# Optimization experiments

Measured on AMD Instinct MI355X. Metric: run time of the kernel, lower is better.

The kernel has to match this reference:

```python
import jax, jax.numpy as jnp
import numpy as np

DIM = 1024          # moe_cfg.dim
INTER = 1024        # moe_cfg.moe_inter_dim
E = 8               # moe_cfg.n_routed_experts
TOPK = 2            # moe_cfg.n_activated_experts
ROUTE_SCALE = 1.0
SHARED_INTER = 2048 # n_shared_experts * moe_inter_dim
B, S = 4, 2048


def setup_inputs() -> dict:
    key = jax.random.key(0)
    ks = jax.random.split(key, 10)
    def w(k, shape, scale=0.02):
        return jax.random.normal(k, shape, jnp.float32) * scale
    return {
        "x": jax.random.normal(ks[0], (B, S, DIM), jnp.float32),
        # Gate (nn.Linear(dim, n_routed_experts, bias=True))
        "gate_w": w(ks[1], (E, DIM)),
        "gate_b": jnp.zeros((E,), jnp.float32),
        # Routed experts, stacked on leading E axis (torch Linear convention: [out, in])
        "w1": w(ks[2], (E, INTER, DIM)), "b1": jnp.zeros((E, INTER), jnp.float32),
        "w3": w(ks[3], (E, INTER, DIM)), "b3": jnp.zeros((E, INTER), jnp.float32),
        "w2": w(ks[4], (E, DIM, INTER)), "b2": jnp.zeros((E, DIM), jnp.float32),
        # Shared expert MLP(dim, n_shared_experts * moe_inter_dim)
        "ws1": w(ks[5], (SHARED_INTER, DIM)), "bs1": jnp.zeros((SHARED_INTER,), jnp.float32),
        "ws3": w(ks[6], (SHARED_INTER, DIM)), "bs3": jnp.zeros((SHARED_INTER,), jnp.float32),
        "ws2": w(ks[7], (DIM, SHARED_INTER)), "bs2": jnp.zeros((DIM,), jnp.float32),
    }


def _moe_forward(x, gate_w, gate_b, w1, b1, w3, b3, w2, b2,
                 ws1, bs1, ws3, bs3, ws2, bs2):
    Bq, Sq, D = x.shape
    xt = x.reshape(-1, D)  # [T, D], T = B*S
    # ---- Gate: softmax scores in fp32, top-k routing (eval mode: no usage buffers) ----
    logits = (xt @ gate_w.T + gate_b).astype(jnp.float32)  # [T, E]
    scores = jax.nn.softmax(logits, axis=-1)
    top_w, top_i = jax.lax.top_k(scores, TOPK)             # values == gathered scores
    weights = (top_w * ROUTE_SCALE).astype(x.dtype)        # [T, topk]
    # Dense combine weights [T, E]: zero for unrouted experts (math identical to dispatch)
    gate_dense = jnp.sum(jax.nn.one_hot(top_i, E, dtype=x.dtype) * weights[..., None], axis=1)
    # ---- Routed experts: SwiGLU FFN per expert (dropout p=0 -> identity) ----
    def expert(w1e, b1e, w3e, b3e, w2e, b2e):
        h = jax.nn.silu(xt @ w1e.T + b1e) * (xt @ w3e.T + b3e)  # [T, INTER]
        return h @ w2e.T + b2e                                   # [T, D]
    outs = jax.vmap(expert)(w1, b1, w3, b3, w2, b2)  # [E, T, D]
    y = jnp.einsum('etd,te->td', outs, gate_dense)   # weighted combine
    # ---- Shared expert MLP (SwiGLU) ----
    z = (jax.nn.silu(xt @ ws1.T + bs1) * (xt @ ws3.T + bs3)) @ ws2.T + bs2
    return (y + z).reshape(Bq, Sq, D)


def reference(x, gate_w, gate_b, w1, b1, w3, b3, w2, b2,
              ws1, bs1, ws3, bs3, ws2, bs2):
    return _moe_forward(x, gate_w, gate_b, w1, b1, w3, b3, w2, b2,
                        ws1, bs1, ws3, bs3, ws2, bs2)
```

## Files before the change

kernel.cpp:

```cpp
#include <hip/hip_runtime.h>
#include <stdint.h>
#include <stddef.h>

#define T_TOK  8192
#define DIMK   1024
#define INTERK 1024
#define NEXP   8
#define SINT   2048
#define CAP    18432
#define RT256  72

typedef float  f32x4  __attribute__((ext_vector_type(4)));
typedef short  bf16x8 __attribute__((ext_vector_type(8)));

typedef __attribute__((address_space(1))) const unsigned int gas_u32;
typedef __attribute__((address_space(3))) unsigned int las_u32;

__device__ __forceinline__ void gload16(const void* g, void* l) {
  __builtin_amdgcn_global_load_lds((gas_u32*)g, (las_u32*)l, 16, 0, 0);
}

__device__ __forceinline__ unsigned short f2b(float f) {
  unsigned int u = __float_as_uint(f);
  u = (u + 0x7FFFu + ((u >> 16) & 1u)) >> 16;
  return (unsigned short)u;
}
__device__ __forceinline__ float b2f(unsigned short h) {
  return __uint_as_float(((unsigned int)h) << 16);
}

__device__ __forceinline__ void barrier_nodrain() {
  asm volatile("" ::: "memory");
  __builtin_amdgcn_s_barrier();
  asm volatile("" ::: "memory");
}

__global__ __launch_bounds__(256) void cvt_kernel(const float4* __restrict__ in,
                                                  unsigned short* __restrict__ out, int n4) {
  int i = blockIdx.x * 256 + threadIdx.x;
  if (i >= n4) return;
  float4 v = in[i];
  ushort4 o;
  o.x = f2b(v.x); o.y = f2b(v.y); o.z = f2b(v.z); o.w = f2b(v.w);
  *reinterpret_cast<ushort4*>(&out[(size_t)i * 4]) = o;
}

template <int ROWS_PER_E, int K4>
__global__ __launch_bounds__(256) void cvt_w13_kernel(
    const float4* __restrict__ w1, const float4* __restrict__ w3,
    unsigned short* __restrict__ out, int n ) {
  int idx = blockIdx.x * 256 + threadIdx.x;
  int is3 = idx >= n;
  int i = is3 ? idx - n : idx;
  if (i >= n) return;
  int r  = i / K4;
  int kc = i - r * K4;
  int e  = r / ROWS_PER_E;
  int rr = r - e * ROWS_PER_E;
  int g  = rr >> 4;
  size_t dst_r = (size_t)e * (2 * ROWS_PER_E) + g * 32 + (is3 ? 16 : 0) + (rr & 15);
  float4 v = (is3 ? w3 : w1)[i];
  ushort4 o;
  o.x = f2b(v.x); o.y = f2b(v.y); o.z = f2b(v.z); o.w = f2b(v.w);
  *reinterpret_cast<ushort4*>(&out[(dst_r * K4 + kc) * 4]) = o;
}

__global__ __launch_bounds__(256) void gate_kernel(
    const float* __restrict__ x, const float* __restrict__ gw, const float* __restrict__ gb,
    int* __restrict__ top_i, float* __restrict__ top_w) {
  int t    = blockIdx.x * 4 + (threadIdx.x >> 6);
  int lane = threadIdx.x & 63;
  const float* xr = x + (size_t)t * DIMK;
  float acc[NEXP];
#pragma unroll
  for (int e = 0; e < NEXP; ++e) acc[e] = 0.f;
  for (int i = lane; i < DIMK; i += 64) {
    float xv = xr[i];
#pragma unroll
    for (int e = 0; e < NEXP; ++e) acc[e] += xv * gw[e * DIMK + i];
  }
#pragma unroll
  for (int e = 0; e < NEXP; ++e) {
    float v = acc[e];
#pragma unroll
    for (int off = 32; off > 0; off >>= 1) v += __shfl_down(v, off, 64);
    acc[e] = v;
  }
  if (lane == 0) {
    float lg[NEXP];
#pragma unroll
    for (int e = 0; e < NEXP; ++e) lg[e] = acc[e] + gb[e];
    int i0 = 0;
#pragma unroll
    for (int e = 1; e < NEXP; ++e) if (lg[e] > lg[i0]) i0 = e;
    int i1 = (i0 == 0) ? 1 : 0;
#pragma unroll
    for (int e = 0; e < NEXP; ++e) if (e != i0 && lg[e] > lg[i1]) i1 = e;
    float mx = lg[i0], s = 0.f;
#pragma unroll
    for (int e = 0; e < NEXP; ++e) s += expf(lg[e] - mx);
    top_i[t * 2]     = i0;
    top_i[t * 2 + 1] = i1;
    top_w[t * 2]     = expf(lg[i0] - mx) / s;
    top_w[t * 2 + 1] = expf(lg[i1] - mx) / s;
  }
}

__global__ __launch_bounds__(512) void route_build_kernel(
    const int* __restrict__ top_i, int* __restrict__ order, int* __restrict__ pos,
    int* __restrict__ poff_g) {
  __shared__ int cnt[NEXP][512];
  __shared__ int base[NEXP][512];
  __shared__ int totals[NEXP];
  __shared__ int poff_s[NEXP + 1];
  int tid = threadIdx.x;
  int lane = tid & 63, w = tid >> 6;
  const int t0 = tid * 16;

  int c[NEXP];
#pragma unroll
  for (int e = 0; e < NEXP; ++e) c[e] = 0;
  for (int j = 0; j < 16; ++j) {
    int e0 = top_i[(t0 + j) * 2];
    int e1 = top_i[(t0 + j) * 2 + 1];
#pragma unroll
    for (int e = 0; e < NEXP; ++e) c[e] += (e0 == e) + (e1 == e);
  }
#pragma unroll
  for (int e = 0; e < NEXP; ++e) cnt[e][tid] = c[e];
  __syncthreads();

  {
    int running = 0;
    for (int ch = 0; ch < 8; ++ch) {
      int v = cnt[w][ch * 64 + lane];
      int incl = v;
#pragma unroll
      for (int off = 1; off < 64; off <<= 1) {
        int u = __shfl_up(incl, off, 64);
        if (lane >= off) incl += u;
      }
      base[w][ch * 64 + lane] = running + incl - v;
      running += __shfl(incl, 63, 64);
    }
    if (lane == 0) totals[w] = running;
  }
  __syncthreads();

  if (tid == 0) {
    int off = 0;
#pragma unroll
    for (int e = 0; e < NEXP; ++e) {
      poff_s[e] = off;
      off += (totals[e] + 255) & ~255;
    }
    poff_s[NEXP] = off;
#pragma unroll
    for (int e = 0; e <= NEXP; ++e) poff_g[e] = poff_s[e];
  }
  __syncthreads();

  int cur[NEXP];
#pragma unroll
  for (int e = 0; e < NEXP; ++e) cur[e] = poff_s[e] + base[e][tid];
  for (int j = 0; j < 16; ++j) {
    int t = t0 + j;
#pragma unroll
    for (int k = 0; k < 2; ++k) {
      int ei = top_i[t * 2 + k];
      int p = 0;
#pragma unroll
      for (int e = 0; e < NEXP; ++e)
        if (ei == e) { p = cur[e]; cur[e] = p + 1; }
      order[p]       = t;
      pos[t * 2 + k] = p;
    }
  }

#pragma unroll
  for (int e = 0; e < NEXP; ++e) {
    int s = poff_s[e] + totals[e], en = poff_s[e + 1];
    for (int i = s + tid; i < en; i += 512) order[i] = 0;
  }
}

#define A_ELE   16384
#define B_ELE   8192
#define BUF_ELE (A_ELE + B_ELE)
template <bool EXPERTS, bool GATHER, int EPI>
__global__ __launch_bounds__(512) void gemm256_kernel(
    const unsigned short* __restrict__ A, int lda,
    const int* __restrict__ order, const int* __restrict__ poff,
    const unsigned short* __restrict__ B,
    const float* __restrict__ bias1, const float* __restrict__ bias3,
    size_t wstride, int bstride, int K,
    void* __restrict__ outp, int ldo) {
  __shared__ unsigned short lds[3 * BUF_ELE];

  int rowbase = blockIdx.y * 256;
  int expert  = 0;
  if (EXPERTS) {
    if (rowbase >= poff[NEXP]) return;
    while (expert < NEXP - 1 && rowbase >= poff[expert + 1]) ++expert;
  }
  const unsigned short* Be = B + (size_t)expert * wstride;

  int tid = threadIdx.x;
  int lane = tid & 63, wid = tid >> 6;
  int wr = wid >> 1, wc = wid & 1;
  int ncolbase = blockIdx.x * 128;

  size_t aoff[4], boff[2];
#pragma unroll
  for (int l = 0; l < 4; ++l) {
    int g = l * 512 + tid;
    int r = g >> 3;
    int sub = (g & 7) ^ (r & 7);
    int gr = GATHER ? order[rowbase + r] : (rowbase + r);
    aoff[l] = (size_t)gr * lda + (size_t)(sub * 8);
  }
#pragma unroll
  for (int l = 0; l < 2; ++l) {
    int g = l * 512 + tid;
    int r = g >> 3;
    int sub = (g & 7) ^ (r & 7);
    boff[l] = (size_t)(ncolbase + r) * K + (size_t)(sub * 8);
  }

  f32x4 acc[4][4];
#pragma unroll
  for (int m = 0; m < 4; ++m)
#pragma unroll
    for (int n = 0; n < 4; ++n) acc[m][n] = f32x4{0.f, 0.f, 0.f, 0.f};

  const int NT = K >> 6;

#pragma unroll
  for (int l = 0; l < 4; ++l)
    gload16(A + aoff[l], &lds[(size_t)(l * 512 + tid) * 8]);
#pragma unroll
  for (int l = 0; l < 2; ++l)
    gload16(Be + boff[l], &lds[A_ELE + (size_t)(l * 512 + tid) * 8]);
#pragma unroll
  for (int l = 0; l < 4; ++l)
    gload16(A + aoff[l] + 64, &lds[BUF_ELE + (size_t)(l * 512 + tid) * 8]);
#pragma unroll
  for (int l = 0; l < 2; ++l)
    gload16(Be + boff[l] + 64, &lds[BUF_ELE + A_ELE + (size_t)(l * 512 + tid) * 8]);

  unsigned int off_r = 0, off_m = BUF_ELE, off_w = 2 * BUF_ELE;

  for (int t = 0; t < NT; ++t) {
    if (t + 1 < NT) {
      asm volatile("s_waitcnt vmcnt(6)" ::: "memory");
    } else {
      asm volatile("s_waitcnt vmcnt(0)" ::: "memory");
    }
    asm volatile("s_waitcnt lgkmcnt(0)" ::: "memory");
    barrier_nodrain();

    const unsigned short* Ab = &lds[off_r];
    const unsigned short* Bb = &lds[off_r + A_ELE];
    const bool stage = (t + 2 < NT);
    const int kb = (t + 2) << 6;

    {
      bf16x8 a[4], b[4];
#pragma unroll
      for (int m = 0; m < 4; ++m) {
        int ra = wr * 64 + m * 16 + (lane & 15);
        int sa = ((lane >> 4)) ^ (ra & 7);
        a[m] = *(const bf16x8*)&Ab[ra * 64 + sa * 8];
      }
#pragma unroll
      for (int n = 0; n < 4; ++n) {
        int rb = wc * 64 + n * 16 + (lane & 15);
        int sb = ((lane >> 4)) ^ (rb & 7);
        b[n] = *(const bf16x8*)&Bb[rb * 64 + sb * 8];
      }
      if (stage) {
#pragma unroll
        for (int l = 0; l < 4; ++l)
          gload16(A + aoff[l] + kb, &lds[off_w + (size_t)(l * 512 + tid) * 8]);
      }
      __builtin_amdgcn_s_setprio(1);
#pragma unroll
      for (int m = 0; m < 4; ++m)
#pragma unroll
        for (int n = 0; n < 4; ++n)
          acc[m][n] = __builtin_amdgcn_mfma_f32_16x16x32_bf16(a[m], b[n], acc[m][n], 0, 0, 0);
      __builtin_amdgcn_s_setprio(0);
    }
    {
      bf16x8 a[4], b[4];
#pragma unroll
      for (int m = 0; m < 4; ++m) {
        int ra = wr * 64 + m * 16 + (lane & 15);
        int sa = (4 + (lane >> 4)) ^ (ra & 7);
        a[m] = *(const bf16x8*)&Ab[ra * 64 + sa * 8];
      }
#pragma unroll
      for (int n = 0; n < 4; ++n) {
        int rb = wc * 64 + n * 16 + (lane & 15);
        int sb = (4 + (lane >> 4)) ^ (rb & 7);
        b[n] = *(const bf16x8*)&Bb[rb * 64 + sb * 8];
      }
      if (stage) {
#pragma unroll
        for (int l = 0; l < 2; ++l)
          gload16(Be + boff[l] + kb, &lds[off_w + A_ELE + (size_t)(l * 512 + tid) * 8]);
      }
      __builtin_amdgcn_s_setprio(1);
#pragma unroll
      for (int m = 0; m < 4; ++m)
#pragma unroll
        for (int n = 0; n < 4; ++n)
          acc[m][n] = __builtin_amdgcn_mfma_f32_16x16x32_bf16(a[m], b[n], acc[m][n], 0, 0, 0);
      __builtin_amdgcn_s_setprio(0);
    }

    unsigned int tmp = off_r; off_r = off_m; off_m = off_w; off_w = tmp;
  }

  if (EPI == 0) {
#pragma unroll
    for (int m = 0; m < 4; ++m)
#pragma unroll
      for (int np = 0; np < 2; ++np) {
        int realcol = (ncolbase >> 1) + wc * 32 + np * 16 + (lane & 15);
        float bb1 = bias1[bstride * expert + realcol];
        float bb3 = bias3[bstride * expert + realcol];
#pragma unroll
        for (int j = 0; j < 4; ++j) {
          int row  = rowbase + wr * 64 + m * 16 + (lane >> 4) * 4 + j;
          float a1 = acc[m][2 * np][j] + bb1;
          float a3 = acc[m][2 * np + 1][j] + bb3;
          float hv = (a1 / (1.f + __expf(-a1))) * a3;
          ((unsigned short*)outp)[(size_t)row * ldo + realcol] = f2b(hv);
        }
      }
  } else {
#pragma unroll
    for (int m = 0; m < 4; ++m)
#pragma unroll
      for (int n = 0; n < 4; ++n) {
        int col  = ncolbase + wc * 64 + n * 16 + (lane & 15);
        float bb = bias1[bstride * expert + col];
#pragma unroll
        for (int j = 0; j < 4; ++j) {
          int row = rowbase + wr * 64 + m * 16 + (lane >> 4) * 4 + j;
          float v = acc[m][n][j] + bb;
          if (EPI == 2)
            ((float*)outp)[(size_t)row * ldo + col] = v;
          else
            ((unsigned short*)outp)[(size_t)row * ldo + col] = f2b(v);
        }
      }
  }
}

__global__ __launch_bounds__(256) void combine_kernel(
    float* __restrict__ out, const unsigned short* __restrict__ y,
    const int* __restrict__ pos, const float* __restrict__ tw) {
  size_t idx = (size_t)blockIdx.x * 256 + threadIdx.x;
  if (idx >= (size_t)T_TOK * DIMK) return;
  int t = (int)(idx >> 10);
  int d = (int)(idx & 1023);
  int p0 = pos[t * 2], p1 = pos[t * 2 + 1];
  float w0 = tw[t * 2], w1 = tw[t * 2 + 1];
  out[idx] += w0 * b2f(y[(size_t)p0 * DIMK + d]) + w1 * b2f(y[(size_t)p1 * DIMK + d]);
}

extern "C" void kernel_launch(void* const* d_in, const int* in_sizes, int n_in,
                              void* d_out, int out_size, void* d_ws, size_t ws_size,
                              hipStream_t stream) {
  const float* x   = (const float*)d_in[0];
  const float* gw  = (const float*)d_in[1];
  const float* gb  = (const float*)d_in[2];
  const float* w1  = (const float*)d_in[3];
  const float* b1  = (const float*)d_in[4];
  const float* w3  = (const float*)d_in[5];
  const float* b3  = (const float*)d_in[6];
  const float* w2  = (const float*)d_in[7];
  const float* b2  = (const float*)d_in[8];
  const float* ws1 = (const float*)d_in[9];
  const float* bs1 = (const float*)d_in[10];
  const float* ws3 = (const float*)d_in[11];
  const float* bs3 = (const float*)d_in[12];
  const float* ws2 = (const float*)d_in[13];
  const float* bs2 = (const float*)d_in[14];
  float* out = (float*)d_out;
  (void)in_sizes; (void)n_in; (void)out_size; (void)ws_size;

  char* p = (char*)d_ws;
  auto alloc = [&](size_t bytes) -> void* {
    void* r = (void*)p;
    p += (bytes + 255) & ~(size_t)255;
    return r;
  };
  unsigned short* xb    = (unsigned short*)alloc((size_t)T_TOK * DIMK * 2);
  unsigned short* w13r  = (unsigned short*)alloc((size_t)NEXP * 2 * INTERK * DIMK * 2);
  unsigned short* w2b   = (unsigned short*)alloc((size_t)NEXP * DIMK * INTERK * 2);
  unsigned short* w13s  = (unsigned short*)alloc((size_t)2 * SINT * DIMK * 2);
  unsigned short* ws2b  = (unsigned short*)alloc((size_t)DIMK * SINT * 2);
  unsigned short* h     = (unsigned short*)alloc((size_t)CAP * INTERK * 2);
  unsigned short* yb    = (unsigned short*)alloc((size_t)CAP * DIMK * 2);
  unsigned short* hs    = (unsigned short*)alloc((size_t)T_TOK * SINT * 2);
  int*   top_i  = (int*)alloc((size_t)T_TOK * 2 * 4);
  float* top_w  = (float*)alloc((size_t)T_TOK * 2 * 4);
  int*   pos    = (int*)alloc((size_t)T_TOK * 2 * 4);
  int*   order  = (int*)alloc((size_t)CAP * 4);
  int*   poff   = (int*)alloc(64);

  auto cvt = [&](const float* src, unsigned short* dst, size_t n) {
    int n4 = (int)(n / 4);
    cvt_kernel<<<(n4 + 255) / 256, 256, 0, stream>>>((const float4*)src, dst, n4);
  };
  cvt(x,   xb,   (size_t)T_TOK * DIMK);
  cvt(w2,  w2b,  (size_t)NEXP * DIMK * INTERK);
  cvt(ws2, ws2b, (size_t)DIMK * SINT);

  {
    int n = NEXP * INTERK * (DIMK / 4);
    cvt_w13_kernel<INTERK, DIMK / 4><<<(2 * n + 255) / 256, 256, 0, stream>>>(
        (const float4*)w1, (const float4*)w3, w13r, n);
  }
  {
    int n = SINT * (DIMK / 4);
    cvt_w13_kernel<SINT, DIMK / 4><<<(2 * n + 255) / 256, 256, 0, stream>>>(
        (const float4*)ws1, (const float4*)ws3, w13s, n);
  }

  gate_kernel<<<T_TOK / 4, 256, 0, stream>>>(x, gw, gb, top_i, top_w);
  route_build_kernel<<<1, 512, 0, stream>>>(top_i, order, pos, poff);

  gemm256_kernel<true, true, 0><<<dim3((2 * INTERK) / 128, RT256), 512, 0, stream>>>(
      xb, DIMK, order, poff, w13r, b1, b3,
      (size_t)2 * INTERK * DIMK, INTERK, DIMK, h, INTERK);
  gemm256_kernel<true, false, 1><<<dim3(DIMK / 128, RT256), 512, 0, stream>>>(
      h, INTERK, (const int*)nullptr, poff, w2b, b2, (const float*)nullptr,
      (size_t)DIMK * INTERK, DIMK, INTERK, (void*)yb, DIMK);

  gemm256_kernel<false, false, 0><<<dim3((2 * SINT) / 128, T_TOK / 256), 512, 0, stream>>>(
      xb, DIMK, (const int*)nullptr, (const int*)nullptr, w13s, bs1, bs3,
      (size_t)0, 0, DIMK, hs, SINT);
  gemm256_kernel<false, false, 2><<<dim3(DIMK / 128, T_TOK / 256), 512, 0, stream>>>(
      hs, SINT, (const int*)nullptr, (const int*)nullptr, ws2b, bs2, (const float*)nullptr,
      (size_t)0, 0, SINT, (void*)out, DIMK);

  combine_kernel<<<(T_TOK * DIMK) / 256, 256, 0, stream>>>(out, yb, pos, top_w);
}
```

Baseline: 397.8 us.

## Restructure GEMM inner loop into two phases split by M with extra barriers

```diff
diff --git a/kernel.cpp b/kernel.cpp
--- a/kernel.cpp
+++ b/kernel.cpp
@@ -256,7 +256,6 @@
     } else {
       asm volatile("s_waitcnt vmcnt(0)" ::: "memory");
     }
-    asm volatile("s_waitcnt lgkmcnt(0)" ::: "memory");
     barrier_nodrain();
 
     const unsigned short* Ab = &lds[off_r];
@@ -264,60 +263,73 @@
     const bool stage = (t + 2 < NT);
     const int kb = (t + 2) << 6;
 
-    {
-      bf16x8 a[4], b[4];
-#pragma unroll
-      for (int m = 0; m < 4; ++m) {
-        int ra = wr * 64 + m * 16 + (lane & 15);
-        int sa = ((lane >> 4)) ^ (ra & 7);
-        a[m] = *(const bf16x8*)&Ab[ra * 64 + sa * 8];
-      }
-#pragma unroll
-      for (int n = 0; n < 4; ++n) {
-        int rb = wc * 64 + n * 16 + (lane & 15);
-        int sb = ((lane >> 4)) ^ (rb & 7);
-        b[n] = *(const bf16x8*)&Bb[rb * 64 + sb * 8];
-      }
-      if (stage) {
-#pragma unroll
-        for (int l = 0; l < 4; ++l)
-          gload16(A + aoff[l] + kb, &lds[off_w + (size_t)(l * 512 + tid) * 8]);
-      }
-      __builtin_amdgcn_s_setprio(1);
-#pragma unroll
-      for (int m = 0; m < 4; ++m)
-#pragma unroll
-        for (int n = 0; n < 4; ++n)
-          acc[m][n] = __builtin_amdgcn_mfma_f32_16x16x32_bf16(a[m], b[n], acc[m][n], 0, 0, 0);
-      __builtin_amdgcn_s_setprio(0);
-    }
-    {
-      bf16x8 a[4], b[4];
-#pragma unroll
-      for (int m = 0; m < 4; ++m) {
-        int ra = wr * 64 + m * 16 + (lane & 15);
-        int sa = (4 + (lane >> 4)) ^ (ra & 7);
-        a[m] = *(const bf16x8*)&Ab[ra * 64 + sa * 8];
-      }
-#pragma unroll
-      for (int n = 0; n < 4; ++n) {
-        int rb = wc * 64 + n * 16 + (lane & 15);
-        int sb = (4 + (lane >> 4)) ^ (rb & 7);
-        b[n] = *(const bf16x8*)&Bb[rb * 64 + sb * 8];
-      }
-      if (stage) {
-#pragma unroll
-        for (int l = 0; l < 2; ++l)
-          gload16(Be + boff[l] + kb, &lds[off_w + A_ELE + (size_t)(l * 512 + tid) * 8]);
-      }
-      __builtin_amdgcn_s_setprio(1);
-#pragma unroll
-      for (int m = 0; m < 4; ++m)
-#pragma unroll
-        for (int n = 0; n < 4; ++n)
-          acc[m][n] = __builtin_amdgcn_mfma_f32_16x16x32_bf16(a[m], b[n], acc[m][n], 0, 0, 0);
-      __builtin_amdgcn_s_setprio(0);
-    }
+    bf16x8 bfr[4][2];
+#pragma unroll
+    for (int n = 0; n < 4; ++n) {
+      int rb = wc * 64 + n * 16 + (lane & 15);
+#pragma unroll
+      for (int kk = 0; kk < 2; ++kk) {
+        int sb = (kk * 4 + (lane >> 4)) ^ (rb & 7);
+        bfr[n][kk] = *(const bf16x8*)&Bb[rb * 64 + sb * 8];
+      }
+    }
+    bf16x8 a0[2][2];
+#pragma unroll
+    for (int m = 0; m < 2; ++m) {
+      int ra = wr * 64 + m * 16 + (lane & 15);
+#pragma unroll
+      for (int kk = 0; kk < 2; ++kk) {
+        int sa = (kk * 4 + (lane >> 4)) ^ (ra & 7);
+        a0[m][kk] = *(const bf16x8*)&Ab[ra * 64 + sa * 8];
+      }
+    }
+    if (stage) {
+#pragma unroll
+      for (int l = 0; l < 3; ++l)
+        gload16(A + aoff[l] + kb, &lds[off_w + (size_t)(l * 512 + tid) * 8]);
+    }
+    barrier_nodrain();
+    asm volatile("s_waitcnt lgkmcnt(0)" ::: "memory");
+    __builtin_amdgcn_sched_barrier(0);
+    __builtin_amdgcn_s_setprio(1);
+#pragma unroll
+    for (int m = 0; m < 2; ++m)
+#pragma unroll
+      for (int n = 0; n < 4; ++n)
+#pragma unroll
+        for (int kk = 0; kk < 2; ++kk)
+          acc[m][n] = __builtin_amdgcn_mfma_f32_16x16x32_bf16(a0[m][kk], bfr[n][kk], acc[m][n], 0, 0, 0);
+    __builtin_amdgcn_s_setprio(0);
+    barrier_nodrain();
+
+    bf16x8 a1[2][2];
+#pragma unroll
+    for (int m = 0; m < 2; ++m) {
+      int ra = wr * 64 + (m + 2) * 16 + (lane & 15);
+#pragma unroll
+      for (int kk = 0; kk < 2; ++kk) {
+        int sa = (kk * 4 + (lane >> 4)) ^ (ra & 7);
+        a1[m][kk] = *(const bf16x8*)&Ab[ra * 64 + sa * 8];
+      }
+    }
+    if (stage) {
+      gload16(A + aoff[3] + kb, &lds[off_w + (size_t)(3 * 512 + tid) * 8]);
+#pragma unroll
+      for (int l = 0; l < 2; ++l)
+        gload16(Be + boff[l] + kb, &lds[off_w + A_ELE + (size_t)(l * 512 + tid) * 8]);
+    }
+    barrier_nodrain();
+    asm volatile("s_waitcnt lgkmcnt(0)" ::: "memory");
+    __builtin_amdgcn_sched_barrier(0);
+    __builtin_amdgcn_s_setprio(1);
+#pragma unroll
+    for (int m = 0; m < 2; ++m)
+#pragma unroll
+      for (int n = 0; n < 4; ++n)
+#pragma unroll
+        for (int kk = 0; kk < 2; ++kk)
+          acc[m + 2][n] = __builtin_amdgcn_mfma_f32_16x16x32_bf16(a1[m][kk], bfr[n][kk], acc[m + 2][n], 0, 0, 0);
+    __builtin_amdgcn_s_setprio(0);
 
     unsigned int tmp = off_r; off_r = off_m; off_m = off_w; off_w = tmp;
   }
```

Result: slower. 411.1 us (+3.3%).

## Merge routed and shared expert GEMMs into two combined launches with XCD-aware block mapping

Applied to the files above, without the earlier changes.

```diff
diff --git a/kernel.cpp b/kernel.cpp
--- a/kernel.cpp
+++ b/kernel.cpp
@@ -9,6 +9,15 @@
 #define SINT   2048
 #define CAP    18432
 #define RT256  72
+
+#define NS1_R  16
+#define NS1_S  32
+#define RT_S   32
+#define G1R    (NS1_R * RT256)
+#define G1     (G1R + NS1_S * RT_S)
+#define NS2    8
+#define G2R    (NS2 * RT256)
+#define G2     (G2R + NS2 * RT_S)
 
 typedef float  f32x4  __attribute__((ext_vector_type(4)));
 typedef short  bf16x8 __attribute__((ext_vector_type(8)));
@@ -187,28 +196,18 @@
 #define A_ELE   16384
 #define B_ELE   8192
 #define BUF_ELE (A_ELE + B_ELE)
-template <bool EXPERTS, bool GATHER, int EPI>
-__global__ __launch_bounds__(512) void gemm256_kernel(
-    const unsigned short* __restrict__ A, int lda,
-    const int* __restrict__ order, const int* __restrict__ poff,
-    const unsigned short* __restrict__ B,
-    const float* __restrict__ bias1, const float* __restrict__ bias3,
-    size_t wstride, int bstride, int K,
-    void* __restrict__ outp, int ldo) {
-  __shared__ unsigned short lds[3 * BUF_ELE];
-
-  int rowbase = blockIdx.y * 256;
-  int expert  = 0;
-  if (EXPERTS) {
-    if (rowbase >= poff[NEXP]) return;
-    while (expert < NEXP - 1 && rowbase >= poff[expert + 1]) ++expert;
-  }
-  const unsigned short* Be = B + (size_t)expert * wstride;
-
+
+template <bool SWIGLU>
+__device__ __forceinline__ void gemm_core(
+    const unsigned short* __restrict__ A, int lda, int K,
+    const int* __restrict__ order, bool gather, int rowbase,
+    const unsigned short* __restrict__ Be,
+    const float* __restrict__ bias1e, const float* __restrict__ bias3e,
+    int ncolbase, void* __restrict__ outp, int ldo, bool outf32,
+    unsigned short* lds) {
   int tid = threadIdx.x;
   int lane = tid & 63, wid = tid >> 6;
   int wr = wid >> 1, wc = wid & 1;
-  int ncolbase = blockIdx.x * 128;
 
   size_t aoff[4], boff[2];
 #pragma unroll
@@ -216,7 +215,7 @@
     int g = l * 512 + tid;
     int r = g >> 3;
     int sub = (g & 7) ^ (r & 7);
-    int gr = GATHER ? order[rowbase + r] : (rowbase + r);
+    int gr = gather ? order[rowbase + r] : (rowbase + r);
     aoff[l] = (size_t)gr * lda + (size_t)(sub * 8);
   }
 #pragma unroll
@@ -261,7 +260,7 @@
 
     const unsigned short* Ab = &lds[off_r];
     const unsigned short* Bb = &lds[off_r + A_ELE];
-    const bool stage = (t + 2 < NT);
+    const bool st = (t + 2 < NT);
     const int kb = (t + 2) << 6;
 
     {
@@ -278,7 +277,7 @@
         int sb = ((lane >> 4)) ^ (rb & 7);
         b[n] = *(const bf16x8*)&Bb[rb * 64 + sb * 8];
       }
-      if (stage) {
+      if (st) {
 #pragma unroll
         for (int l = 0; l < 4; ++l)
           gload16(A + aoff[l] + kb, &lds[off_w + (size_t)(l * 512 + tid) * 8]);
@@ -305,7 +304,7 @@
         int sb = (4 + (lane >> 4)) ^ (rb & 7);
         b[n] = *(const bf16x8*)&Bb[rb * 64 + sb * 8];
       }
-      if (stage) {
+      if (st) {
 #pragma unroll
         for (int l = 0; l < 2; ++l)
           gload16(Be + boff[l] + kb, &lds[off_w + A_ELE + (size_t)(l * 512 + tid) * 8]);
@@ -322,14 +321,14 @@
     unsigned int tmp = off_r; off_r = off_m; off_m = off_w; off_w = tmp;
   }
 
-  if (EPI == 0) {
+  if (SWIGLU) {
 #pragma unroll
     for (int m = 0; m < 4; ++m)
 #pragma unroll
       for (int np = 0; np < 2; ++np) {
         int realcol = (ncolbase >> 1) + wc * 32 + np * 16 + (lane & 15);
-        float bb1 = bias1[bstride * expert + realcol];
-        float bb3 = bias3[bstride * expert + realcol];
+        float bb1 = bias1e[realcol];
+        float bb3 = bias3e[realcol];
 #pragma unroll
         for (int j = 0; j < 4; ++j) {
           int row  = rowbase + wr * 64 + m * 16 + (lane >> 4) * 4 + j;
@@ -345,17 +344,79 @@
 #pragma unroll
       for (int n = 0; n < 4; ++n) {
         int col  = ncolbase + wc * 64 + n * 16 + (lane & 15);
-        float bb = bias1[bstride * expert + col];
+        float bb = bias1e[col];
 #pragma unroll
         for (int j = 0; j < 4; ++j) {
           int row = rowbase + wr * 64 + m * 16 + (lane >> 4) * 4 + j;
           float v = acc[m][n][j] + bb;
-          if (EPI == 2)
+          if (outf32)
             ((float*)outp)[(size_t)row * ldo + col] = v;
           else
             ((unsigned short*)outp)[(size_t)row * ldo + col] = f2b(v);
         }
       }
+  }
+}
+
+__global__ __launch_bounds__(512) void gemm1m_kernel(
+    const unsigned short* __restrict__ xb,
+    const int* __restrict__ order, const int* __restrict__ poff,
+    const unsigned short* __restrict__ w13r,
+    const float* __restrict__ b1, const float* __restrict__ b3,
+    const unsigned short* __restrict__ w13s,
+    const float* __restrict__ bs1, const float* __restrict__ bs3,
+    unsigned short* __restrict__ h, unsigned short* __restrict__ hs) {
+  __shared__ unsigned short lds[3 * BUF_ELE];
+
+  int raw = blockIdx.x;
+  int id  = (raw & 7) * (G1 / 8) + (raw >> 3);
+
+  if (id < G1R) {
+    int by = id / NS1_R, bx = id - by * NS1_R;
+    int rowbase = by * 256;
+    if (rowbase >= poff[NEXP]) return;
+    int expert = 0;
+    while (expert < NEXP - 1 && rowbase >= poff[expert + 1]) ++expert;
+    gemm_core<true>(xb, DIMK, DIMK, order, true, rowbase,
+                    w13r + (size_t)expert * 2 * INTERK * DIMK,
+                    b1 + expert * INTERK, b3 + expert * INTERK,
+                    bx * 128, (void*)h, INTERK, false, lds);
+  } else {
+    int id2 = id - G1R;
+    int by = id2 / NS1_S, bx = id2 - by * NS1_S;
+    gemm_core<true>(xb, DIMK, DIMK, (const int*)nullptr, false, by * 256,
+                    w13s, bs1, bs3,
+                    bx * 128, (void*)hs, SINT, false, lds);
+  }
+}
+
+__global__ __launch_bounds__(512) void gemm2m_kernel(
+    const unsigned short* __restrict__ h, const unsigned short* __restrict__ hs,
+    const int* __restrict__ poff,
+    const unsigned short* __restrict__ w2b, const float* __restrict__ b2,
+    const unsigned short* __restrict__ ws2b, const float* __restrict__ bs2,
+    unsigned short* __restrict__ yb, float* __restrict__ out) {
+  __shared__ unsigned short lds[3 * BUF_ELE];
+
+  int raw = blockIdx.x;
+  int id  = (raw & 7) * (G2 / 8) + (raw >> 3);
+
+  if (id < G2R) {
+    int by = id / NS2, bx = id - by * NS2;
+    int rowbase = by * 256;
+    if (rowbase >= poff[NEXP]) return;
+    int expert = 0;
+    while (expert < NEXP - 1 && rowbase >= poff[expert + 1]) ++expert;
+    gemm_core<false>(h, INTERK, INTERK, (const int*)nullptr, false, rowbase,
+                     w2b + (size_t)expert * DIMK * INTERK,
+                     b2 + expert * DIMK, (const float*)nullptr,
+                     bx * 128, (void*)yb, DIMK, false, lds);
+  } else {
+    int id2 = id - G2R;
+    int by = id2 / NS2, bx = id2 - by * NS2;
+    gemm_core<false>(hs, SINT, SINT, (const int*)nullptr, false, by * 256,
+                     ws2b, bs2, (const float*)nullptr,
+                     bx * 128, (void*)out, DIMK, true, lds);
   }
 }
 
@@ -434,19 +495,9 @@
   gate_kernel<<<T_TOK / 4, 256, 0, stream>>>(x, gw, gb, top_i, top_w);
   route_build_kernel<<<1, 512, 0, stream>>>(top_i, order, pos, poff);
 
-  gemm256_kernel<true, true, 0><<<dim3((2 * INTERK) / 128, RT256), 512, 0, stream>>>(
-      xb, DIMK, order, poff, w13r, b1, b3,
-      (size_t)2 * INTERK * DIMK, INTERK, DIMK, h, INTERK);
-  gemm256_kernel<true, false, 1><<<dim3(DIMK / 128, RT256), 512, 0, stream>>>(
-      h, INTERK, (const int*)nullptr, poff, w2b, b2, (const float*)nullptr,
-      (size_t)DIMK * INTERK, DIMK, INTERK, (void*)yb, DIMK);
-
-  gemm256_kernel<false, false, 0><<<dim3((2 * SINT) / 128, T_TOK / 256), 512, 0, stream>>>(
-      xb, DIMK, (const int*)nullptr, (const int*)nullptr, w13s, bs1, bs3,
-      (size_t)0, 0, DIMK, hs, SINT);
-  gemm256_kernel<false, false, 2><<<dim3(DIMK / 128, T_TOK / 256), 512, 0, stream>>>(
-      hs, SINT, (const int*)nullptr, (const int*)nullptr, ws2b, bs2, (const float*)nullptr,
-      (size_t)0, 0, SINT, (void*)out, DIMK);
+  gemm1m_kernel<<<G1, 512, 0, stream>>>(xb, order, poff, w13r, b1, b3,
+                                        w13s, bs1, bs3, h, hs);
+  gemm2m_kernel<<<G2, 512, 0, stream>>>(h, hs, poff, w2b, b2, ws2b, bs2, yb, out);
 
   combine_kernel<<<(T_TOK * DIMK) / 256, 256, 0, stream>>>(out, yb, pos, top_w);
 }
```

Result: no change. 394.2 us (-0.9%).
